# Kernel tuning notes

Measured on AMD Instinct MI355X. Metric: run time of the kernel, lower is better.

Reference implementation:

```python
import jax, jax.numpy as jnp
import numpy as np

N_NODES = 30000
N_EDGES = 480000
EMB_DIM = 512
NUM_REL = 4
VOCAB = 64


def setup_inputs() -> dict:
    key = jax.random.key(0)
    ks = jax.random.split(key, 14)

    def nrm(k, shape):
        return jax.random.normal(k, shape, dtype=jnp.float32) * 0.05

    return {
        "x_idx": jax.random.randint(ks[0], (N_NODES, 1), 0, VOCAB),
        "edge_index": jax.random.randint(ks[1], (2, N_EDGES), 0, N_NODES),
        "edge_type": jax.random.randint(ks[2], (N_EDGES,), 0, NUM_REL),
        "emb": nrm(ks[3], (VOCAB, EMB_DIM)),
        "W1": nrm(ks[4], (NUM_REL, EMB_DIM, EMB_DIM)),
        "root1": nrm(ks[5], (EMB_DIM, EMB_DIM)),
        "b1": jnp.zeros((EMB_DIM,), jnp.float32),
        "W2": nrm(ks[6], (NUM_REL, EMB_DIM, EMB_DIM)),
        "root2": nrm(ks[7], (EMB_DIM, EMB_DIM)),
        "b2": jnp.zeros((EMB_DIM,), jnp.float32),
        "W3": nrm(ks[8], (NUM_REL, EMB_DIM, EMB_DIM)),
        "root3": nrm(ks[9], (EMB_DIM, EMB_DIM)),
        "b3": jnp.zeros((EMB_DIM,), jnp.float32),
    }


def rgcn_conv(x, src, dst, etype, W, Wroot, b):
    # PyG RGCNConv semantics: per-relation MEAN aggregation of neighbor
    # features, transformed by relation weight, plus root transform + bias.
    # Aggregate-then-transform is mathematically identical to per-edge
    # transform (mean is linear) but needs only R dense GEMMs.
    R = W.shape[0]
    Nn, Dd = x.shape
    seg = etype * Nn + dst  # combined (relation, dst) segment id
    msg_sum = jax.ops.segment_sum(x[src], seg, num_segments=R * Nn)
    msg_sum = msg_sum.reshape(R, Nn, Dd)  # [R, N, D]
    cnt = jax.ops.segment_sum(jnp.ones((src.shape[0],), x.dtype), seg,
                              num_segments=R * Nn).reshape(R, Nn, 1)
    mean = msg_sum / jnp.maximum(cnt, 1.0)  # zero rows stay zero
    out = jnp.einsum('rnd,rde->ne', mean, W)  # relation-specific transform
    return out + x @ Wroot + b


def reference(x_idx, edge_index, edge_type, emb,
              W1, root1, b1, W2, root2, b2, W3, root3, b3):
    src, dst = edge_index[0], edge_index[1]
    x = emb[x_idx[:, 0]]  # [N, D] embedding lookup (squeeze(-1))
    x = jax.nn.relu(rgcn_conv(x, src, dst, edge_type, W1, root1, b1)) + x
    x = jax.nn.relu(rgcn_conv(x, src, dst, edge_type, W2, root2, b2)) + x
    x = jax.nn.relu(rgcn_conv(x, src, dst, edge_type, W3, root3, b3)) + x
    return x
```

## Files before the change

kernel.cpp:

```cpp
#include <hip/hip_runtime.h>
#include <hip/hip_bf16.h>

#define N_NODES 30000
#define N_EDGES 480000
#define DIM 512
#define NREL 4
#define NSEG (NREL * N_NODES)
#define KTOT ((NREL + 1) * DIM)
#define NT (KTOT / 64)
#define NBM ((N_NODES + 255) / 256)
#define NWG_GEMM (NBM * 2)

typedef __attribute__((ext_vector_type(8))) short short8;
typedef __attribute__((ext_vector_type(4))) float f32x4;

__device__ __forceinline__ float bf2f(unsigned int hi) {
    union { unsigned int u; float f; } v; v.u = hi << 16; return v.f;
}
__device__ __forceinline__ unsigned short f2bf(float f) {
    union { float f; unsigned int u; } v; v.f = f;
    unsigned int u = v.u;
    unsigned int r = (u + 0x7fffu + ((u >> 16) & 1u)) >> 16;
    return (unsigned short)r;
}

__global__ void k_wcat(const float* __restrict__ W, const float* __restrict__ root,
                       unsigned short* __restrict__ wt) {
    int i = blockIdx.x * 256 + threadIdx.x;
    if (i >= DIM * KTOT) return;
    int k = i % KTOT, e = i / KTOT;
    float v;
    if (k < DIM) {
        v = root[k * DIM + e];
    } else {
        int kk = k - DIM;
        int r = kk >> 9; kk &= 511;
        v = W[(size_t)r * DIM * DIM + (size_t)kk * DIM + e];
    }
    wt[(size_t)e * KTOT + k] = f2bf(v);
}

__global__ void k_embed(const int* __restrict__ xidx, const float* __restrict__ emb,
                        unsigned short* __restrict__ xb) {
    int n = blockIdx.x;
    int l = threadIdx.x;
    int id = xidx[n];
    const float4* er = (const float4*)(emb + (size_t)id * DIM + l * 8);
    float4 a = er[0], b = er[1];
    ushort4 pa, pb;
    pa.x = f2bf(a.x); pa.y = f2bf(a.y); pa.z = f2bf(a.z); pa.w = f2bf(a.w);
    pb.x = f2bf(b.x); pb.y = f2bf(b.y); pb.z = f2bf(b.z); pb.w = f2bf(b.w);
    ushort4* xbo = (ushort4*)(xb + (size_t)n * DIM + l * 8);
    xbo[0] = pa; xbo[1] = pb;
}

__global__ void k_hist(const int* __restrict__ etype, const int* __restrict__ dst,
                       int* __restrict__ hist) {
    int e = blockIdx.x * 256 + threadIdx.x;
    if (e < N_EDGES) atomicAdd(&hist[etype[e] * N_NODES + dst[e]], 1);
}

__global__ void k_scan1(const int* __restrict__ hist, int* __restrict__ offsets,
                        int* __restrict__ bsums) {
    __shared__ int sdata[256];
    int t = threadIdx.x, b = blockIdx.x;
    int base = b * 2048 + t * 8;
    int v[8]; int s = 0;
    #pragma unroll
    for (int i = 0; i < 8; i++) {
        int idx = base + i;
        v[i] = (idx < NSEG) ? hist[idx] : 0;
        s += v[i];
    }
    sdata[t] = s; __syncthreads();
    for (int off = 1; off < 256; off <<= 1) {
        int x = (t >= off) ? sdata[t - off] : 0;
        __syncthreads();
        sdata[t] += x;
        __syncthreads();
    }
    int run = (t == 0) ? 0 : sdata[t - 1];
    #pragma unroll
    for (int i = 0; i < 8; i++) {
        run += v[i];
        int idx = base + i;
        if (idx < NSEG) offsets[idx + 1] = run;
    }
    if (t == 255) bsums[b] = sdata[255];
}

__global__ void k_scan2(int* __restrict__ bsums, int nb) {
    if (threadIdx.x == 0 && blockIdx.x == 0) {
        int run = 0;
        for (int i = 0; i < nb; i++) { int v = bsums[i]; bsums[i] = run; run += v; }
    }
}

__global__ void k_scan3(const int* __restrict__ bsums, int* __restrict__ offsets) {
    int t = threadIdx.x, b = blockIdx.x;
    int base = b * 2048 + t * 8;
    int add = bsums[b];
    #pragma unroll
    for (int i = 0; i < 8; i++) {
        int idx = base + i;
        if (idx < NSEG) offsets[idx + 1] += add;
    }
    if (b == 0 && t == 0) offsets[0] = 0;
}

__global__ void k_scatter(const int* __restrict__ etype, const int* __restrict__ src,
                          const int* __restrict__ dst, const int* __restrict__ offsets,
                          int* __restrict__ cursor, int* __restrict__ ssrc) {
    int e = blockIdx.x * 256 + threadIdx.x;
    if (e < N_EDGES) {
        int seg = etype[e] * N_NODES + dst[e];
        int p = atomicAdd(&cursor[seg], 1);
        ssrc[offsets[seg] + p] = src[e];
    }
}

__global__ __launch_bounds__(256) void k_agg(const unsigned short* __restrict__ xb,
                                             const int* __restrict__ ssrc,
                                             const int* __restrict__ offsets,
                                             unsigned short* __restrict__ meanb) {
    int wid = threadIdx.x >> 6, lane = threadIdx.x & 63;
    int seg = blockIdx.x * 4 + wid;
    int st = offsets[seg], en = offsets[seg + 1];
    float acc[8] = {0, 0, 0, 0, 0, 0, 0, 0};
    int i = st;
    for (; i + 1 < en; i += 2) {
        int s0 = ssrc[i], s1 = ssrc[i + 1];
        uint4 v0 = *(const uint4*)(xb + (size_t)s0 * DIM + lane * 8);
        uint4 v1 = *(const uint4*)(xb + (size_t)s1 * DIM + lane * 8);
        acc[0] += bf2f(v0.x & 0xffffu) + bf2f(v1.x & 0xffffu);
        acc[1] += bf2f(v0.x >> 16)     + bf2f(v1.x >> 16);
        acc[2] += bf2f(v0.y & 0xffffu) + bf2f(v1.y & 0xffffu);
        acc[3] += bf2f(v0.y >> 16)     + bf2f(v1.y >> 16);
        acc[4] += bf2f(v0.z & 0xffffu) + bf2f(v1.z & 0xffffu);
        acc[5] += bf2f(v0.z >> 16)     + bf2f(v1.z >> 16);
        acc[6] += bf2f(v0.w & 0xffffu) + bf2f(v1.w & 0xffffu);
        acc[7] += bf2f(v0.w >> 16)     + bf2f(v1.w >> 16);
    }
    if (i < en) {
        int s = ssrc[i];
        uint4 v = *(const uint4*)(xb + (size_t)s * DIM + lane * 8);
        acc[0] += bf2f(v.x & 0xffffu); acc[1] += bf2f(v.x >> 16);
        acc[2] += bf2f(v.y & 0xffffu); acc[3] += bf2f(v.y >> 16);
        acc[4] += bf2f(v.z & 0xffffu); acc[5] += bf2f(v.z >> 16);
        acc[6] += bf2f(v.w & 0xffffu); acc[7] += bf2f(v.w >> 16);
    }
    float inv = (en > st) ? 1.0f / (float)(en - st) : 0.0f;
    uint4 o;
    o.x = (unsigned int)f2bf(acc[0] * inv) | ((unsigned int)f2bf(acc[1] * inv) << 16);
    o.y = (unsigned int)f2bf(acc[2] * inv) | ((unsigned int)f2bf(acc[3] * inv) << 16);
    o.z = (unsigned int)f2bf(acc[4] * inv) | ((unsigned int)f2bf(acc[5] * inv) << 16);
    o.w = (unsigned int)f2bf(acc[6] * inv) | ((unsigned int)f2bf(acc[7] * inv) << 16);
    *(uint4*)(meanb + (size_t)seg * DIM + lane * 8) = o;
}


#define GLD16(g, l)                                                                     \
    __builtin_amdgcn_global_load_lds((const __attribute__((address_space(1))) void*)(g), \
                                     (__attribute__((address_space(3))) void*)(l), 16, 0, 0)

#define STAGE_A(tile, ksh, bufo) do {                                                   \
    int _pt = (tile) >> 3;                                                              \
    const unsigned short* _ab = (_pt == 0) ? xb : meanb + (size_t)(_pt - 1) * N_NODES * DIM; \
    int _kc = (((tile) & 7) << 6) + ((ksh) << 5) + gcol;         \
    int _g0 = m0 + srow; if (_g0 >= N_NODES) _g0 = 0;                                   \
    int _g1 = m0 + srow + 128; if (_g1 >= N_NODES) _g1 = 0;                             \
    GLD16(_ab + (size_t)_g0 * DIM + _kc, S + (bufo) + ((ksh) * 8192) + (wid << 9));     \
    GLD16(_ab + (size_t)_g1 * DIM + _kc, S + (bufo) + ((ksh) * 8192) + 4096 + (wid << 9)); \
} while (0)

#define STAGE_B(tile, ksh, bufo) do {                                                   \
    int _kc = ((tile) << 6) + ((ksh) << 5) + gcol;                  \
    const unsigned short* _w0 = wt + (size_t)(n0 + srow) * KTOT + _kc;                  \
    GLD16(_w0, S + (bufo) + 16384 + ((ksh) * 8192) + (wid << 9));                       \
    GLD16(_w0 + (size_t)128 * KTOT, S + (bufo) + 16384 + ((ksh) * 8192) + 4096 + (wid << 9)); \
} while (0)

#define READ_A8(ks, bufo) do {                                                          \
    const unsigned short* _ap = S + (bufo) + (ks) * 8192 + arowF + cofs;                \
    a[0] = *(const short8*)(_ap);                                                       \
    a[1] = *(const short8*)(_ap + 512);                                                 \
    a[2] = *(const short8*)(_ap + 1024);                                                \
    a[3] = *(const short8*)(_ap + 1536);                                                \
    a[4] = *(const short8*)(_ap + 2048);                                                \
    a[5] = *(const short8*)(_ap + 2560);                                                \
    a[6] = *(const short8*)(_ap + 3072);                                                \
    a[7] = *(const short8*)(_ap + 3584);                                                \
} while (0)

#define READ_B(ks, bufo) do {                                                           \
    const unsigned short* _bp = S + (bufo) + 16384 + (ks) * 8192 + brow0 + cofs;        \
    b[0] = *(const short8*)(_bp);                                                       \
    b[1] = *(const short8*)(_bp + 512);                                                 \
    b[2] = *(const short8*)(_bp + 1024);                                                \
    b[3] = *(const short8*)(_bp + 1536);                                                \
} while (0)

#define MFMA32() do {                                                                   \
    _Pragma("unroll") for (int _m = 0; _m < 8; ++_m)                                    \
    _Pragma("unroll") for (int _n = 0; _n < 4; ++_n)                                    \
        acc[_m][_n] =                                                                   \
            __builtin_amdgcn_mfma_f32_16x16x32_bf16(a[_m], b[_n], acc[_m][_n], 0, 0, 0); \
} while (0)

#define PH_TOP()  __builtin_amdgcn_s_barrier();                                         \
                  asm volatile("s_waitcnt lgkmcnt(0)" ::: "memory");                    \
                  __builtin_amdgcn_sched_barrier(0);                                    \
                  __builtin_amdgcn_s_setprio(1)
#define PH_BOT()  __builtin_amdgcn_s_setprio(0); __builtin_amdgcn_sched_barrier(0);     \
                  __builtin_amdgcn_s_barrier()
#define VMC4()    asm volatile("s_waitcnt vmcnt(4)" ::: "memory")
#define VMC0()    asm volatile("s_waitcnt vmcnt(0)" ::: "memory")
#define BUF1 32768

__global__ __launch_bounds__(512, 2) void k_gemm(const unsigned short* __restrict__ xb,
                                                 const unsigned short* __restrict__ meanb,
                                                 const unsigned short* __restrict__ wt,
                                                 const float* __restrict__ bias,
                                                 float* __restrict__ outf,
                                                 unsigned short* __restrict__ xbn,
                                                 int wf32, int wbf16) {
    extern __shared__ unsigned short S[];
    int tid = threadIdx.x;
    int lane = tid & 63, wid = tid >> 6;

    int orig = blockIdx.x;
    int xcd = orig & 7, tix = orig >> 3;
    const int q = NWG_GEMM >> 3, r = NWG_GEMM & 7;
    int wgid = (xcd < r ? xcd * (q + 1) : r * (q + 1) + (xcd - r) * q) + tix;
    int bn = wgid & 1, bm = wgid >> 1;
    int m0 = bm * 256, n0 = bn * 256;
    int wm = wid >> 2, wn = wid & 3;

    int r15 = lane & 15, c4 = lane >> 4;
    int f = (r15 + (r15 >> 2)) & 3;
    int cofs = ((c4 ^ f) << 3);
    int arowF = (wm * 128 + r15) * 32;
    int brow0 = (wn * 64 + r15) * 32;

    int srow = tid >> 2;
    int f_t = (srow + (srow >> 2)) & 3;
    int gcol = (((tid & 3) ^ f_t) << 3);

    short8 a[8], b[4];
    f32x4 acc[8][4] = {};

    STAGE_A(0, 0, 0);    STAGE_B(0, 0, 0);
    STAGE_A(0, 1, 0);    STAGE_B(0, 1, 0);
    STAGE_A(1, 0, BUF1); STAGE_B(1, 0, BUF1);
    VMC4();
    __builtin_amdgcn_s_barrier();

    for (int it = 0; it < NT / 2; ++it) {
        int t1 = 2 * it + 1, t2 = 2 * it + 2, t3 = 2 * it + 3;
        READ_A8(0, 0); READ_B(0, 0);
        STAGE_A(t1, 1, BUF1); STAGE_B(t1, 1, BUF1);
        PH_TOP(); MFMA32(); PH_BOT();
        READ_A8(1, 0); READ_B(1, 0);
        if (t2 < NT) { STAGE_A(t2, 0, 0); STAGE_B(t2, 0, 0); VMC4(); } else { VMC0(); }
        PH_TOP(); MFMA32(); PH_BOT();
        READ_A8(0, BUF1); READ_B(0, BUF1);
        if (t2 < NT) { STAGE_A(t2, 1, 0); STAGE_B(t2, 1, 0); }
        PH_TOP(); MFMA32(); PH_BOT();
        READ_A8(1, BUF1); READ_B(1, BUF1);
        if (t3 < NT) { STAGE_A(t3, 0, BUF1); STAGE_B(t3, 0, BUF1); VMC4(); } else { VMC0(); }
        PH_TOP(); MFMA32(); PH_BOT();
    }
    VMC0();

    #pragma unroll
    for (int mm = 0; mm < 8; ++mm) {
        int rowoff = ((mm >> 2) << 6) + ((mm & 3) << 4);
        #pragma unroll
        for (int j = 0; j < 4; ++j) {
            int row = m0 + wm * 128 + rowoff + c4 * 4 + j;
            if (row >= N_NODES) continue;
            #pragma unroll
            for (int n = 0; n < 4; ++n) {
                int col = n0 + wn * 64 + n * 16 + r15;
                float v = acc[mm][n][j] + bias[col];
                v = fmaxf(v, 0.0f) + bf2f(xb[(size_t)row * DIM + col]);
                if (wf32)  outf[(size_t)row * DIM + col] = v;
                if (wbf16) xbn[(size_t)row * DIM + col] = f2bf(v);
            }
        }
    }
}

extern "C" void kernel_launch(void* const* d_in, const int* in_sizes, int n_in,
                              void* d_out, int out_size, void* d_ws, size_t ws_size,
                              hipStream_t stream) {
    const int* xidx   = (const int*)d_in[0];
    const int* eidx   = (const int*)d_in[1];
    const int* etype  = (const int*)d_in[2];
    const float* emb  = (const float*)d_in[3];
    const float* Wl[3]    = {(const float*)d_in[4], (const float*)d_in[7], (const float*)d_in[10]};
    const float* rootl[3] = {(const float*)d_in[5], (const float*)d_in[8], (const float*)d_in[11]};
    const float* bl[3]    = {(const float*)d_in[6], (const float*)d_in[9], (const float*)d_in[12]};
    const int* esrc = eidx;
    const int* edst = eidx + N_EDGES;

    char* ws = (char*)d_ws;
    size_t off = 0;
    auto take = [&](size_t bytes) { char* p = ws + off; off = (off + bytes + 255) & ~(size_t)255; return p; };
    unsigned short* xb0  = (unsigned short*)take((size_t)N_NODES * DIM * 2);
    unsigned short* xb1  = (unsigned short*)take((size_t)N_NODES * DIM * 2);
    unsigned short* meanb= (unsigned short*)take((size_t)NREL * N_NODES * DIM * 2);
    unsigned short* wcat = (unsigned short*)take((size_t)3 * DIM * KTOT * 2);
    int* hist    = (int*)take((size_t)NSEG * 4);
    int* offsets = (int*)take((size_t)(NSEG + 1) * 4);
    int* cursor  = (int*)take((size_t)NSEG * 4);
    int* bsums   = (int*)take(64 * 4);
    int* ssrc    = (int*)take((size_t)N_EDGES * 4);

    hipMemsetAsync(hist, 0, (size_t)NSEG * 4, stream);
    hipMemsetAsync(cursor, 0, (size_t)NSEG * 4, stream);
    for (int l = 0; l < 3; l++) {
        k_wcat<<<(DIM * KTOT + 255) / 256, 256, 0, stream>>>(Wl[l], rootl[l],
                                                             wcat + (size_t)l * DIM * KTOT);
    }
    k_embed<<<N_NODES, 64, 0, stream>>>(xidx, emb, xb0);
    k_hist<<<(N_EDGES + 255) / 256, 256, 0, stream>>>(etype, edst, hist);
    k_scan1<<<(NSEG + 2047) / 2048, 256, 0, stream>>>(hist, offsets, bsums);
    k_scan2<<<1, 64, 0, stream>>>(bsums, (NSEG + 2047) / 2048);
    k_scan3<<<(NSEG + 2047) / 2048, 256, 0, stream>>>(bsums, offsets);
    k_scatter<<<(N_EDGES + 255) / 256, 256, 0, stream>>>(etype, esrc, edst, offsets, cursor, ssrc);

    unsigned short* xb_cur = xb0;
    unsigned short* xb_nxt = xb1;
    for (int l = 0; l < 3; l++) {
        k_agg<<<N_NODES, 256, 0, stream>>>(xb_cur, ssrc, offsets, meanb);
        int last = (l == 2);
        k_gemm<<<NWG_GEMM, 512, 131072, stream>>>(xb_cur, meanb, wcat + (size_t)l * DIM * KTOT,
                                                  bl[l], (float*)d_out, xb_nxt,
                                                  last ? 1 : 0, last ? 0 : 1);
        unsigned short* t = xb_cur; xb_cur = xb_nxt; xb_nxt = t;
    }
}
```

Before: 659.1 us.

## Merge weight-prep launches and relax GEMM LDS wait/sched barriers

The three per-layer weight concatenate/convert kernels become one launch with a 3-deep grid dimension, removing two launches. In the GEMM main loop, the explicit lgkmcnt(0) wait and sched_barriers around each MFMA phase are removed, and B fragments are read from LDS before A fragments. This leaves the compiler to place LDS waits and may let MFMAs start on partially arrived operands. The cost is less control over instruction scheduling, which could cause stalls or hurt the hand-tuned interleave.

```diff
diff --git a/kernel.cpp b/kernel.cpp
--- a/kernel.cpp
+++ b/kernel.cpp
@@ -24,8 +24,14 @@
     return (unsigned short)r;
 }
 
-__global__ void k_wcat(const float* __restrict__ W, const float* __restrict__ root,
-                       unsigned short* __restrict__ wt) {
+__global__ void k_wcat3(const float* __restrict__ W0, const float* __restrict__ r0,
+                        const float* __restrict__ W1, const float* __restrict__ r1,
+                        const float* __restrict__ W2, const float* __restrict__ r2,
+                        unsigned short* __restrict__ wt) {
+    int l = blockIdx.y;
+    const float* W    = (l == 0) ? W0 : (l == 1) ? W1 : W2;
+    const float* root = (l == 0) ? r0 : (l == 1) ? r1 : r2;
+    unsigned short* o = wt + (size_t)l * DIM * KTOT;
     int i = blockIdx.x * 256 + threadIdx.x;
     if (i >= DIM * KTOT) return;
     int k = i % KTOT, e = i / KTOT;
@@ -37,7 +43,7 @@
         int r = kk >> 9; kk &= 511;
         v = W[(size_t)r * DIM * DIM + (size_t)kk * DIM + e];
     }
-    wt[(size_t)e * KTOT + k] = f2bf(v);
+    o[(size_t)e * KTOT + k] = f2bf(v);
 }
 
 __global__ void k_embed(const int* __restrict__ xidx, const float* __restrict__ emb,
@@ -207,12 +213,8 @@
             __builtin_amdgcn_mfma_f32_16x16x32_bf16(a[_m], b[_n], acc[_m][_n], 0, 0, 0); \
 } while (0)
 
-#define PH_TOP()  __builtin_amdgcn_s_barrier();                                         \
-                  asm volatile("s_waitcnt lgkmcnt(0)" ::: "memory");                    \
-                  __builtin_amdgcn_sched_barrier(0);                                    \
-                  __builtin_amdgcn_s_setprio(1)
-#define PH_BOT()  __builtin_amdgcn_s_setprio(0); __builtin_amdgcn_sched_barrier(0);     \
-                  __builtin_amdgcn_s_barrier()
+#define PH_TOP()  __builtin_amdgcn_s_barrier(); __builtin_amdgcn_s_setprio(1)
+#define PH_BOT()  __builtin_amdgcn_s_setprio(0); __builtin_amdgcn_s_barrier()
 #define VMC4()    asm volatile("s_waitcnt vmcnt(4)" ::: "memory")
 #define VMC0()    asm volatile("s_waitcnt vmcnt(0)" ::: "memory")
 #define BUF1 32768
@@ -257,16 +259,16 @@
 
     for (int it = 0; it < NT / 2; ++it) {
         int t1 = 2 * it + 1, t2 = 2 * it + 2, t3 = 2 * it + 3;
-        READ_A8(0, 0); READ_B(0, 0);
+        READ_B(0, 0); READ_A8(0, 0);
         STAGE_A(t1, 1, BUF1); STAGE_B(t1, 1, BUF1);
         PH_TOP(); MFMA32(); PH_BOT();
-        READ_A8(1, 0); READ_B(1, 0);
+        READ_B(1, 0); READ_A8(1, 0);
         if (t2 < NT) { STAGE_A(t2, 0, 0); STAGE_B(t2, 0, 0); VMC4(); } else { VMC0(); }
         PH_TOP(); MFMA32(); PH_BOT();
-        READ_A8(0, BUF1); READ_B(0, BUF1);
+        READ_B(0, BUF1); READ_A8(0, BUF1);
         if (t2 < NT) { STAGE_A(t2, 1, 0); STAGE_B(t2, 1, 0); }
         PH_TOP(); MFMA32(); PH_BOT();
-        READ_A8(1, BUF1); READ_B(1, BUF1);
+        READ_B(1, BUF1); READ_A8(1, BUF1);
         if (t3 < NT) { STAGE_A(t3, 0, BUF1); STAGE_B(t3, 0, BUF1); VMC4(); } else { VMC0(); }
         PH_TOP(); MFMA32(); PH_BOT();
     }
@@ -319,10 +321,8 @@
 
     hipMemsetAsync(hist, 0, (size_t)NSEG * 4, stream);
     hipMemsetAsync(cursor, 0, (size_t)NSEG * 4, stream);
-    for (int l = 0; l < 3; l++) {
-        k_wcat<<<(DIM * KTOT + 255) / 256, 256, 0, stream>>>(Wl[l], rootl[l],
-                                                             wcat + (size_t)l * DIM * KTOT);
-    }
+    dim3 wg((DIM * KTOT + 255) / 256, 3);
+    k_wcat3<<<wg, 256, 0, stream>>>(Wl[0], rootl[0], Wl[1], rootl[1], Wl[2], rootl[2], wcat);
     k_embed<<<N_NODES, 64, 0, stream>>>(xidx, emb, xb0);
     k_hist<<<(N_EDGES + 255) / 256, 256, 0, stream>>>(etype, edst, hist);
     k_scan1<<<(NSEG + 2047) / 2048, 256, 0, stream>>>(hist, offsets, bsums);
```

Measured after the change: 765.2 us. +16.1%, slower.
